# Kernel tuning notes

Measured on AMD Instinct MI355X. Metric: run time of the kernel, lower is better.

The kernel has to match this reference:

```python
import jax, jax.numpy as jnp
import numpy as np
from jax import lax

B, T, K = 8192, 512, 5


def setup_inputs() -> dict:
    key = jax.random.key(0)
    k1, k2, k3, k4 = jax.random.split(key, 4)
    potentials = jax.random.normal(k1, (B, T, K), dtype=jnp.float32)
    transition_params = jax.random.normal(k2, (K, K), dtype=jnp.float32) * 0.1
    sequence_lengths = jax.random.randint(k3, (B,), 1, T + 1, dtype=jnp.int32)
    tag_indices = jax.random.randint(k4, (B, T), 0, K, dtype=jnp.int32)
    return {
        "potentials": potentials,
        "transition_params": transition_params,
        "sequence_lengths": sequence_lengths,
        "tag_indices": tag_indices,
    }


def _crf(potentials, transition_params, sequence_lengths, tag_indices):
    Bn, Tn, Kn = potentials.shape
    alpha0 = potentials[:, 0]                        # (B, K)
    pots_rest = jnp.swapaxes(potentials[:, 1:], 0, 1)  # (T-1, B, K)
    ts = jnp.arange(1, Tn)
    valid = ts[:, None] < sequence_lengths[None, :]    # (T-1, B)
    tag_range = jnp.arange(Kn, dtype=jnp.int32)

    # ---- Viterbi forward: max-product DP with backpointers ----
    def vit_step(alpha, inp):
        pot_t, v = inp
        scores = alpha[:, :, None] + transition_params[None]  # (B, K, K) over prev i -> next j
        bp = jnp.argmax(scores, axis=1).astype(jnp.int32)     # (B, K)
        new_alpha = jnp.max(scores, axis=1) + pot_t
        alpha = jnp.where(v[:, None], new_alpha, alpha)       # freeze past seq end
        bp = jnp.where(v[:, None], bp, tag_range[None])       # identity bp past seq end
        return alpha, bp

    alpha_v, bps = lax.scan(vit_step, alpha0, (pots_rest, valid))
    last_tag = jnp.argmax(alpha_v, axis=1).astype(jnp.int32)  # (B,)

    # ---- backtrack ----
    def back_step(tag, bp_t):
        prev = jnp.take_along_axis(bp_t, tag[:, None], axis=1)[:, 0]
        return prev, prev

    _, prev_tags = lax.scan(back_step, last_tag, bps, reverse=True)  # (T-1, B) tags 0..T-2
    decoded = jnp.concatenate([jnp.swapaxes(prev_tags, 0, 1), last_tag[:, None]], axis=1)
    mask = jnp.arange(Tn)[None] < sequence_lengths[:, None]          # (B, T)
    decoded = jnp.where(mask, decoded, 0)

    # ---- forward algorithm: log partition ----
    def fwd_step(alpha, inp):
        pot_t, v = inp
        new_alpha = jax.nn.logsumexp(alpha[:, :, None] + transition_params[None], axis=1) + pot_t
        return jnp.where(v[:, None], new_alpha, alpha), None

    alpha_f, _ = lax.scan(fwd_step, alpha0, (pots_rest, valid))
    log_norm = jax.nn.logsumexp(alpha_f, axis=1)                     # (B,)

    # ---- gold sequence score ----
    unary = jnp.take_along_axis(potentials, tag_indices[:, :, None], axis=2)[:, :, 0]  # (B, T)
    unary = jnp.sum(jnp.where(mask, unary, 0.0), axis=1)
    trans_sc = transition_params[tag_indices[:, :-1], tag_indices[:, 1:]]              # (B, T-1)
    tmask = jnp.arange(1, Tn)[None] < sequence_lengths[:, None]
    binary = jnp.sum(jnp.where(tmask, trans_sc, 0.0), axis=1)

    log_likelihood = unary + binary - log_norm
    return decoded, log_likelihood


def reference(potentials, transition_params, sequence_lengths, tag_indices):
    return _crf(potentials, transition_params, sequence_lengths, tag_indices)
```

## Files before the change

kernel.cpp:

```cpp
#include <hip/hip_runtime.h>
#include <stdint.h>

#define KK 5
#define TT 512

template<int P> __device__ __forceinline__ float swzf(float v) {
  return __int_as_float(__builtin_amdgcn_ds_swizzle(__float_as_int(v), P));
}
template<int P> __device__ __forceinline__ int swzi(int v) {
  return __builtin_amdgcn_ds_swizzle(v, P);
}
#define BC0 0x018
#define BC1 0x038
#define BC2 0x058
#define BC3 0x078
#define BC4 0x098
#define X1 0x041F
#define X2 0x081F
#define X4 0x101F

__device__ __forceinline__ float sel5f(float v0,float v1,float v2,float v3,float v4,int ct){
  float u=v0; u=(ct==1)?v1:u; u=(ct==2)?v2:u; u=(ct==3)?v3:u; u=(ct==4)?v4:u; return u;
}
__device__ __forceinline__ uint32_t sel5u(uint32_t w0,uint32_t w1,uint32_t w2,uint32_t w3,uint32_t w4,int ct){
  uint32_t u=w0; u=(ct==1)?w1:u; u=(ct==2)?w2:u; u=(ct==3)?w3:u; u=(ct==4)?w4:u; return u;
}
__device__ __forceinline__ int telt(const int4 (&tp)[2], int s) {
  const int4 v = (s < 4) ? tp[0] : tp[1];
  const int m = s & 3;
  return m == 0 ? v.x : (m == 1 ? v.y : (m == 2 ? v.z : v.w));
}

__device__ __forceinline__ void loadCol(float (&d)[8], const float* __restrict__ colp, int k) {
  const int t0 = k * 8 + 1;
  if (k < TT / 8 - 1) {
#pragma unroll
    for (int s = 0; s < 8; ++s) d[s] = colp[(t0 + s) * KK];
  } else {
#pragma unroll
    for (int s = 0; s < 8; ++s) d[s] = colp[min(t0 + s, TT - 1) * KK];
  }
}
__device__ __forceinline__ void loadTag(int4 (&tp)[2], const int* __restrict__ tg, int k) {
  tp[0] = *(const int4*)(tg + 8 * k);
  tp[1] = *(const int4*)(tg + 8 * k + 4);
}

__global__ void sort_by_len(const int* __restrict__ lens, int* __restrict__ order, int B) {
  __shared__ int hist[513];
  __shared__ int off[513];
  const int tid = threadIdx.x;
  for (int i = tid; i < 513; i += 1024) hist[i] = 0;
  __syncthreads();
  for (int b = tid; b < B; b += 1024) atomicAdd(&hist[lens[b]], 1);
  __syncthreads();
  if (tid < 64) {
    int local[9];
    int sum = 0;
#pragma unroll
    for (int j = 0; j < 9; ++j) {
      const int i = tid * 9 + j;
      const int v = (i < 513) ? hist[i] : 0;
      local[j] = sum;
      sum += v;
    }
    int inc = sum;
#pragma unroll
    for (int d = 1; d < 64; d <<= 1) {
      const int n = __shfl_up(inc, d);
      inc += (tid >= d) ? n : 0;
    }
    const int excl = inc - sum;
#pragma unroll
    for (int j = 0; j < 9; ++j) {
      const int i = tid * 9 + j;
      if (i < 513) off[i] = excl + local[j];
    }
  }
  __syncthreads();
  for (int b = tid; b < B; b += 1024) {
    const int p = atomicAdd(&off[lens[b]], 1);
    order[B - 1 - p] = b;
  }
}

__device__ __forceinline__ void vit_map_block(const float (&pv)[8], int k, int len_eff,
                                              const float (&trc)[KK], float& a,
                                              int jj, int g, int r,
                                              uint32_t* __restrict__ s_map) {
  uint32_t bits = 0;
#pragma unroll
  for (int s = 0; s < 8; ++s) {
    const float av0 = swzf<BC0>(a), av1 = swzf<BC1>(a), av2 = swzf<BC2>(a),
                av3 = swzf<BC3>(a), av4 = swzf<BC4>(a);
    const float s0 = av0 + trc[0], s1 = av1 + trc[1], s2 = av2 + trc[2],
                s3 = av3 + trc[3], s4 = av4 + trc[4];
    const float bm = fmaxf(fmaxf(fmaxf(s0, s1), fmaxf(s2, s3)), s4);
    int bi = 4;
    bi = (s3 == bm) ? 3 : bi;
    bi = (s2 == bm) ? 2 : bi;
    bi = (s1 == bm) ? 1 : bi;
    bi = (s0 == bm) ? 0 : bi;
    const int t = k * 8 + s + 1;
    const bool act = (t < len_eff);
    a = act ? (bm + pv[s]) : a;
    const int bie = act ? bi : jj;
    bits |= (uint32_t)bie << (3 * s);
  }
  const uint32_t w0 = (uint32_t)__builtin_amdgcn_ds_bpermute(((g << 3) + 0) << 2, (int)bits);
  const uint32_t w1 = (uint32_t)__builtin_amdgcn_ds_bpermute(((g << 3) + 1) << 2, (int)bits);
  const uint32_t w2 = (uint32_t)__builtin_amdgcn_ds_bpermute(((g << 3) + 2) << 2, (int)bits);
  const uint32_t w3 = (uint32_t)__builtin_amdgcn_ds_bpermute(((g << 3) + 3) << 2, (int)bits);
  const uint32_t w4 = (uint32_t)__builtin_amdgcn_ds_bpermute(((g << 3) + 4) << 2, (int)bits);
  int cur = jj;
  uint32_t dec = 0;
#pragma unroll
  for (int s = 7; s >= 0; --s) {
    const uint32_t w = sel5u(w0, w1, w2, w3, w4, cur);
    const int b3 = (int)((w >> (3 * s)) & 7u);
    dec |= (uint32_t)b3 << (3 * s);
    cur = b3;
  }
  if (r < 5) s_map[g * 321 + k * 5 + jj] = dec;
}

__device__ __forceinline__ void fwd_blk(const float (&pv)[8], const int4 (&tp)[2],
                                        int k, int len, int len_eff,
                                        const float (&Wc)[KK], const float (&trcR)[KK],
                                        float& p, float& Cacc,
                                        float& pvcar, int& tagcar,
                                        float& usum, float& bsum, int r) {
#pragma unroll
  for (int s = 0; s < 8; ++s) {
    const float p0 = swzf<BC0>(p), p1 = swzf<BC1>(p), p2 = swzf<BC2>(p),
                p3 = swzf<BC3>(p), p4 = swzf<BC4>(p);
    const float u  = fmaf(p1, Wc[1], p0 * Wc[0]);
    const float v2 = fmaf(p3, Wc[3], p2 * Wc[2]);
    const float acc = fmaf(p4, Wc[4], u + v2);
    const float E = __expf(pv[s]);
    const int t = k * 8 + s + 1;
    const bool act = (t < len_eff);
    p = act ? (acc * E) : p;
  }
#pragma unroll
  for (int s2 = 0; s2 < 8; ++s2) {
    const int t = k * 8 + s2;
    const int ct = telt(tp, s2);
    const int pt = (s2 == 0) ? tagcar : telt(tp, s2 - 1);
    const float potv = (s2 == 0) ? pvcar : pv[s2 - 1];
    const bool um = (t < len) && (ct == r);
    usum += um ? potv : 0.0f;
    bsum += (um && t >= 1) ? sel5f(trcR[0], trcR[1], trcR[2], trcR[3], trcR[4], pt) : 0.0f;
  }
  pvcar = pv[7];
  tagcar = telt(tp, 7);
  float m = p;
  m = fmaxf(m, swzf<X1>(m));
  m = fmaxf(m, swzf<X2>(m));
  m = fmaxf(m, swzf<X4>(m));
  p *= (1.0f / m);
  Cacc += __logf(m);
}

__launch_bounds__(64)
__global__ void crf_kernel(const float* __restrict__ pot,
                           const float* __restrict__ trans,
                           const int* __restrict__ lens,
                           const int* __restrict__ tags,
                           const int* __restrict__ order,
                           float* __restrict__ out,
                           int B, int T) {
  __shared__ uint32_t s_map[8 * 321];
  __shared__ uint32_t s_chosen[8 * 65];
  const int lane = threadIdx.x;
  const int g = lane >> 3, r = lane & 7;
  const int jj = (r < 5) ? r : 4;
  const unsigned u = blockIdx.x;
  const int role = (u >> 3) & 1;
  const int idx = (int)((u & 7u) | ((u >> 4) << 3));
  const int b = order[idx * 8 + g];
  const int len = lens[b];
  const int len_eff = (r < 5) ? len : 0;
  const float* __restrict__ prow = pot + (size_t)b * (T * KK);
  const float* __restrict__ colp = prow + jj;

  int ml = len;
  ml = max(ml, __shfl_xor(ml, 8));
  ml = max(ml, __shfl_xor(ml, 16));
  ml = max(ml, __shfl_xor(ml, 32));
  const int nblk = (ml + 7) >> 3;

  if (role == 0) {
    float trc[KK];
#pragma unroll
    for (int i = 0; i < KK; ++i) trc[i] = trans[i * KK + jj];
    float a = (r < 5) ? prow[jj] : -3.0e38f;

    float pA[8], pB[8], pC[8];
    loadCol(pA, colp, 0);
    loadCol(pB, colp, min(1, nblk - 1));
    loadCol(pC, colp, min(2, nblk - 1));
    int blk = 0;
    while (true) {
      vit_map_block(pA, blk, len_eff, trc, a, jj, g, r, s_map);
      if (++blk == nblk) break;
      loadCol(pA, colp, min(blk + 2, nblk - 1));
      vit_map_block(pB, blk, len_eff, trc, a, jj, g, r, s_map);
      if (++blk == nblk) break;
      loadCol(pB, colp, min(blk + 2, nblk - 1));
      vit_map_block(pC, blk, len_eff, trc, a, jj, g, r, s_map);
      if (++blk == nblk) break;
      loadCol(pC, colp, min(blk + 2, nblk - 1));
    }
    float bm = a;
    bm = fmaxf(bm, swzf<X1>(bm));
    bm = fmaxf(bm, swzf<X2>(bm));
    bm = fmaxf(bm, swzf<X4>(bm));
    int cand = (r < 5 && a == bm) ? r : 7;
    cand = min(cand, swzi<X1>(cand));
    cand = min(cand, swzi<X2>(cand));
    cand = min(cand, swzi<X4>(cand));
    const int last = cand;

    if (r == 0) {
      int tag = last;
      for (int k2 = nblk - 1; k2 >= 0; --k2) {
        const uint32_t w = s_map[g * 321 + k2 * 5 + tag];
        s_chosen[g * 65 + k2] = w;
        tag = (int)(w & 7u);
      }
    }

    float* __restrict__ orow = out + (size_t)b * T;
#pragma unroll
    for (int kk = 0; kk < 8; ++kk) {
      const int k2 = kk * 8 + r;
      const uint32_t w = s_chosen[g * 65 + k2];
      const int base = k2 * 8;
      float f[8];
#pragma unroll
      for (int pI = 0; pI < 8; ++pI)
        f[pI] = (base + pI < len) ? (float)((w >> (3 * pI)) & 7u) : 0.0f;
      *(float4*)(orow + base)     = make_float4(f[0], f[1], f[2], f[3]);
      *(float4*)(orow + base + 4) = make_float4(f[4], f[5], f[6], f[7]);
    }

  } else {
    float Wc[KK], trcR[KK];
#pragma unroll
    for (int i = 0; i < KK; ++i) {
      trcR[i] = trans[i * KK + jj];
      Wc[i] = __expf(trcR[i]);
    }
    const float pj0 = prow[jj];
    float p = (r < 5) ? __expf(pj0) : 0.0f;
    float Cacc = 0.0f;
    float usum = 0.0f, bsum = 0.0f;
    float pvcar = pj0;
    int tagcar = 0;
    const int* __restrict__ tg = tags + (size_t)b * T;

    float pA[8], pB[8], pC[8];
    int4 TA[2], TB[2], TC[2];
    loadCol(pA, colp, 0);                loadTag(TA, tg, 0);
    loadCol(pB, colp, min(1, nblk - 1)); loadTag(TB, tg, min(1, nblk - 1));
    loadCol(pC, colp, min(2, nblk - 1)); loadTag(TC, tg, min(2, nblk - 1));
    int blk = 0;
    while (true) {
      fwd_blk(pA, TA, blk, len, len_eff, Wc, trcR, p, Cacc, pvcar, tagcar, usum, bsum, r);
      if (++blk == nblk) break;
      loadCol(pA, colp, min(blk + 2, nblk - 1)); loadTag(TA, tg, min(blk + 2, nblk - 1));
      fwd_blk(pB, TB, blk, len, len_eff, Wc, trcR, p, Cacc, pvcar, tagcar, usum, bsum, r);
      if (++blk == nblk) break;
      loadCol(pB, colp, min(blk + 2, nblk - 1)); loadTag(TB, tg, min(blk + 2, nblk - 1));
      fwd_blk(pC, TC, blk, len, len_eff, Wc, trcR, p, Cacc, pvcar, tagcar, usum, bsum, r);
      if (++blk == nblk) break;
      loadCol(pC, colp, min(blk + 2, nblk - 1)); loadTag(TC, tg, min(blk + 2, nblk - 1));
    }
    float sc = usum + bsum;
    sc += swzf<X1>(sc);
    sc += swzf<X2>(sc);
    sc += swzf<X4>(sc);
    float ps = p;
    ps += swzf<X1>(ps);
    ps += swzf<X2>(ps);
    ps += swzf<X4>(ps);
    const float logZ = Cacc + __logf(ps);
    if (r == 0) out[(size_t)B * T + b] = sc - logZ;
  }
}

extern "C" void kernel_launch(void* const* d_in, const int* in_sizes, int n_in,
                              void* d_out, int out_size, void* d_ws, size_t ws_size,
                              hipStream_t stream) {
  const float* pot   = (const float*)d_in[0];
  const float* trans = (const float*)d_in[1];
  const int*   lens  = (const int*)d_in[2];
  const int*   tags  = (const int*)d_in[3];
  float* out = (float*)d_out;

  const int B = in_sizes[2];
  const int T = in_sizes[3] / B;

  int* order = (int*)d_ws;

  sort_by_len<<<1, 1024, 0, stream>>>(lens, order, B);

  const int nblocks = 2 * (B / 8);
  crf_kernel<<<nblocks, 64, 0, stream>>>(pot, trans, lens, tags, order, out, B, T);
}
```

Measured before the change: 90.88 us.

## Fuse Viterbi and forward-algorithm recurrences into a single wavefront per sequence group

Merges the two roles (Viterbi max-product and forward logsumexp plus gold score) that used to run in separate blocks into one block doing both recurrences in the same time-step loop. Potentials and tags are loaded once instead of twice, and the two independent dependency chains are interleaved to hide swizzle and ALU latency. The grid halves to B/8 blocks, so there is less parallelism and more register pressure per wave.

```diff
diff --git a/kernel.cpp b/kernel.cpp
--- a/kernel.cpp
+++ b/kernel.cpp
@@ -84,15 +84,21 @@
   }
 }
 
-__device__ __forceinline__ void vit_map_block(const float (&pv)[8], int k, int len_eff,
-                                              const float (&trc)[KK], float& a,
-                                              int jj, int g, int r,
-                                              uint32_t* __restrict__ s_map) {
+__device__ __forceinline__ void vf_block(const float (&pv)[8], const int4 (&tp)[2],
+    int k, int len, int len_eff,
+    const float (&trc)[KK], const float (&Wc)[KK],
+    float& aV, float& p, float& Cacc,
+    float& pvcar, int& tagcar, float& usum, float& bsum,
+    int jj, int g, int r, uint32_t* __restrict__ s_map) {
   uint32_t bits = 0;
 #pragma unroll
   for (int s = 0; s < 8; ++s) {
-    const float av0 = swzf<BC0>(a), av1 = swzf<BC1>(a), av2 = swzf<BC2>(a),
-                av3 = swzf<BC3>(a), av4 = swzf<BC4>(a);
+    const float av0 = swzf<BC0>(aV), av1 = swzf<BC1>(aV), av2 = swzf<BC2>(aV),
+                av3 = swzf<BC3>(aV), av4 = swzf<BC4>(aV);
+    const float q0 = swzf<BC0>(p), q1 = swzf<BC1>(p), q2 = swzf<BC2>(p),
+                q3 = swzf<BC3>(p), q4 = swzf<BC4>(p);
+    const int t = k * 8 + s + 1;
+    const bool act = (t < len_eff);
     const float s0 = av0 + trc[0], s1 = av1 + trc[1], s2 = av2 + trc[2],
                 s3 = av3 + trc[3], s4 = av4 + trc[4];
     const float bm = fmaxf(fmaxf(fmaxf(s0, s1), fmaxf(s2, s3)), s4);
@@ -101,12 +107,27 @@
     bi = (s2 == bm) ? 2 : bi;
     bi = (s1 == bm) ? 1 : bi;
     bi = (s0 == bm) ? 0 : bi;
-    const int t = k * 8 + s + 1;
-    const bool act = (t < len_eff);
-    a = act ? (bm + pv[s]) : a;
+    aV = act ? (bm + pv[s]) : aV;
     const int bie = act ? bi : jj;
     bits |= (uint32_t)bie << (3 * s);
-  }
+    const float uacc = fmaf(q1, Wc[1], q0 * Wc[0]);
+    const float v2 = fmaf(q3, Wc[3], q2 * Wc[2]);
+    const float acc = fmaf(q4, Wc[4], uacc + v2);
+    const float E = __expf(pv[s]);
+    p = act ? (acc * E) : p;
+  }
+#pragma unroll
+  for (int s2 = 0; s2 < 8; ++s2) {
+    const int t = k * 8 + s2;
+    const int ct = telt(tp, s2);
+    const int pt = (s2 == 0) ? tagcar : telt(tp, s2 - 1);
+    const float potv = (s2 == 0) ? pvcar : pv[s2 - 1];
+    const bool um = (t < len) && (ct == r);
+    usum += um ? potv : 0.0f;
+    bsum += (um && t >= 1) ? sel5f(trc[0], trc[1], trc[2], trc[3], trc[4], pt) : 0.0f;
+  }
+  pvcar = pv[7];
+  tagcar = telt(tp, 7);
   const uint32_t w0 = (uint32_t)__builtin_amdgcn_ds_bpermute(((g << 3) + 0) << 2, (int)bits);
   const uint32_t w1 = (uint32_t)__builtin_amdgcn_ds_bpermute(((g << 3) + 1) << 2, (int)bits);
   const uint32_t w2 = (uint32_t)__builtin_amdgcn_ds_bpermute(((g << 3) + 2) << 2, (int)bits);
@@ -122,38 +143,6 @@
     cur = b3;
   }
   if (r < 5) s_map[g * 321 + k * 5 + jj] = dec;
-}
-
-__device__ __forceinline__ void fwd_blk(const float (&pv)[8], const int4 (&tp)[2],
-                                        int k, int len, int len_eff,
-                                        const float (&Wc)[KK], const float (&trcR)[KK],
-                                        float& p, float& Cacc,
-                                        float& pvcar, int& tagcar,
-                                        float& usum, float& bsum, int r) {
-#pragma unroll
-  for (int s = 0; s < 8; ++s) {
-    const float p0 = swzf<BC0>(p), p1 = swzf<BC1>(p), p2 = swzf<BC2>(p),
-                p3 = swzf<BC3>(p), p4 = swzf<BC4>(p);
-    const float u  = fmaf(p1, Wc[1], p0 * Wc[0]);
-    const float v2 = fmaf(p3, Wc[3], p2 * Wc[2]);
-    const float acc = fmaf(p4, Wc[4], u + v2);
-    const float E = __expf(pv[s]);
-    const int t = k * 8 + s + 1;
-    const bool act = (t < len_eff);
-    p = act ? (acc * E) : p;
-  }
-#pragma unroll
-  for (int s2 = 0; s2 < 8; ++s2) {
-    const int t = k * 8 + s2;
-    const int ct = telt(tp, s2);
-    const int pt = (s2 == 0) ? tagcar : telt(tp, s2 - 1);
-    const float potv = (s2 == 0) ? pvcar : pv[s2 - 1];
-    const bool um = (t < len) && (ct == r);
-    usum += um ? potv : 0.0f;
-    bsum += (um && t >= 1) ? sel5f(trcR[0], trcR[1], trcR[2], trcR[3], trcR[4], pt) : 0.0f;
-  }
-  pvcar = pv[7];
-  tagcar = telt(tp, 7);
   float m = p;
   m = fmaxf(m, swzf<X1>(m));
   m = fmaxf(m, swzf<X2>(m));
@@ -175,10 +164,7 @@
   const int lane = threadIdx.x;
   const int g = lane >> 3, r = lane & 7;
   const int jj = (r < 5) ? r : 4;
-  const unsigned u = blockIdx.x;
-  const int role = (u >> 3) & 1;
-  const int idx = (int)((u & 7u) | ((u >> 4) << 3));
-  const int b = order[idx * 8 + g];
+  const int b = order[blockIdx.x * 8 + g];
   const int len = lens[b];
   const int len_eff = (r < 5) ? len : 0;
   const float* __restrict__ prow = pot + (size_t)b * (T * KK);
@@ -190,103 +176,80 @@
   ml = max(ml, __shfl_xor(ml, 32));
   const int nblk = (ml + 7) >> 3;
 
-  if (role == 0) {
-    float trc[KK];
-#pragma unroll
-    for (int i = 0; i < KK; ++i) trc[i] = trans[i * KK + jj];
-    float a = (r < 5) ? prow[jj] : -3.0e38f;
-
-    float pA[8], pB[8], pC[8];
-    loadCol(pA, colp, 0);
-    loadCol(pB, colp, min(1, nblk - 1));
-    loadCol(pC, colp, min(2, nblk - 1));
-    int blk = 0;
-    while (true) {
-      vit_map_block(pA, blk, len_eff, trc, a, jj, g, r, s_map);
-      if (++blk == nblk) break;
-      loadCol(pA, colp, min(blk + 2, nblk - 1));
-      vit_map_block(pB, blk, len_eff, trc, a, jj, g, r, s_map);
-      if (++blk == nblk) break;
-      loadCol(pB, colp, min(blk + 2, nblk - 1));
-      vit_map_block(pC, blk, len_eff, trc, a, jj, g, r, s_map);
-      if (++blk == nblk) break;
-      loadCol(pC, colp, min(blk + 2, nblk - 1));
-    }
-    float bm = a;
-    bm = fmaxf(bm, swzf<X1>(bm));
-    bm = fmaxf(bm, swzf<X2>(bm));
-    bm = fmaxf(bm, swzf<X4>(bm));
-    int cand = (r < 5 && a == bm) ? r : 7;
-    cand = min(cand, swzi<X1>(cand));
-    cand = min(cand, swzi<X2>(cand));
-    cand = min(cand, swzi<X4>(cand));
-    const int last = cand;
-
-    if (r == 0) {
-      int tag = last;
-      for (int k2 = nblk - 1; k2 >= 0; --k2) {
-        const uint32_t w = s_map[g * 321 + k2 * 5 + tag];
-        s_chosen[g * 65 + k2] = w;
-        tag = (int)(w & 7u);
-      }
-    }
-
-    float* __restrict__ orow = out + (size_t)b * T;
-#pragma unroll
-    for (int kk = 0; kk < 8; ++kk) {
-      const int k2 = kk * 8 + r;
-      const uint32_t w = s_chosen[g * 65 + k2];
-      const int base = k2 * 8;
-      float f[8];
-#pragma unroll
-      for (int pI = 0; pI < 8; ++pI)
-        f[pI] = (base + pI < len) ? (float)((w >> (3 * pI)) & 7u) : 0.0f;
-      *(float4*)(orow + base)     = make_float4(f[0], f[1], f[2], f[3]);
-      *(float4*)(orow + base + 4) = make_float4(f[4], f[5], f[6], f[7]);
-    }
-
-  } else {
-    float Wc[KK], trcR[KK];
-#pragma unroll
-    for (int i = 0; i < KK; ++i) {
-      trcR[i] = trans[i * KK + jj];
-      Wc[i] = __expf(trcR[i]);
-    }
-    const float pj0 = prow[jj];
-    float p = (r < 5) ? __expf(pj0) : 0.0f;
-    float Cacc = 0.0f;
-    float usum = 0.0f, bsum = 0.0f;
-    float pvcar = pj0;
-    int tagcar = 0;
-    const int* __restrict__ tg = tags + (size_t)b * T;
-
-    float pA[8], pB[8], pC[8];
-    int4 TA[2], TB[2], TC[2];
-    loadCol(pA, colp, 0);                loadTag(TA, tg, 0);
-    loadCol(pB, colp, min(1, nblk - 1)); loadTag(TB, tg, min(1, nblk - 1));
-    loadCol(pC, colp, min(2, nblk - 1)); loadTag(TC, tg, min(2, nblk - 1));
-    int blk = 0;
-    while (true) {
-      fwd_blk(pA, TA, blk, len, len_eff, Wc, trcR, p, Cacc, pvcar, tagcar, usum, bsum, r);
-      if (++blk == nblk) break;
-      loadCol(pA, colp, min(blk + 2, nblk - 1)); loadTag(TA, tg, min(blk + 2, nblk - 1));
-      fwd_blk(pB, TB, blk, len, len_eff, Wc, trcR, p, Cacc, pvcar, tagcar, usum, bsum, r);
-      if (++blk == nblk) break;
-      loadCol(pB, colp, min(blk + 2, nblk - 1)); loadTag(TB, tg, min(blk + 2, nblk - 1));
-      fwd_blk(pC, TC, blk, len, len_eff, Wc, trcR, p, Cacc, pvcar, tagcar, usum, bsum, r);
-      if (++blk == nblk) break;
-      loadCol(pC, colp, min(blk + 2, nblk - 1)); loadTag(TC, tg, min(blk + 2, nblk - 1));
-    }
-    float sc = usum + bsum;
-    sc += swzf<X1>(sc);
-    sc += swzf<X2>(sc);
-    sc += swzf<X4>(sc);
-    float ps = p;
-    ps += swzf<X1>(ps);
-    ps += swzf<X2>(ps);
-    ps += swzf<X4>(ps);
-    const float logZ = Cacc + __logf(ps);
-    if (r == 0) out[(size_t)B * T + b] = sc - logZ;
+  float trc[KK], Wc[KK];
+#pragma unroll
+  for (int i = 0; i < KK; ++i) {
+    trc[i] = trans[i * KK + jj];
+    Wc[i] = __expf(trc[i]);
+  }
+  const float pj0 = prow[jj];
+  float aV = (r < 5) ? pj0 : -3.0e38f;
+  float p = (r < 5) ? __expf(pj0) : 0.0f;
+  float Cacc = 0.0f, usum = 0.0f, bsum = 0.0f;
+  float pvcar = pj0;
+  int tagcar = 0;
+  const int* __restrict__ tg = tags + (size_t)b * T;
+
+  float pA[8], pB[8], pC[8];
+  int4 TA[2], TB[2], TC[2];
+  loadCol(pA, colp, 0);                loadTag(TA, tg, 0);
+  loadCol(pB, colp, min(1, nblk - 1)); loadTag(TB, tg, min(1, nblk - 1));
+  loadCol(pC, colp, min(2, nblk - 1)); loadTag(TC, tg, min(2, nblk - 1));
+  int blk = 0;
+  while (true) {
+    vf_block(pA, TA, blk, len, len_eff, trc, Wc, aV, p, Cacc, pvcar, tagcar, usum, bsum, jj, g, r, s_map);
+    if (++blk == nblk) break;
+    loadCol(pA, colp, min(blk + 2, nblk - 1)); loadTag(TA, tg, min(blk + 2, nblk - 1));
+    vf_block(pB, TB, blk, len, len_eff, trc, Wc, aV, p, Cacc, pvcar, tagcar, usum, bsum, jj, g, r, s_map);
+    if (++blk == nblk) break;
+    loadCol(pB, colp, min(blk + 2, nblk - 1)); loadTag(TB, tg, min(blk + 2, nblk - 1));
+    vf_block(pC, TC, blk, len, len_eff, trc, Wc, aV, p, Cacc, pvcar, tagcar, usum, bsum, jj, g, r, s_map);
+    if (++blk == nblk) break;
+    loadCol(pC, colp, min(blk + 2, nblk - 1)); loadTag(TC, tg, min(blk + 2, nblk - 1));
+  }
+
+  float bm = aV;
+  bm = fmaxf(bm, swzf<X1>(bm));
+  bm = fmaxf(bm, swzf<X2>(bm));
+  bm = fmaxf(bm, swzf<X4>(bm));
+  int cand = (r < 5 && aV == bm) ? r : 7;
+  cand = min(cand, swzi<X1>(cand));
+  cand = min(cand, swzi<X2>(cand));
+  cand = min(cand, swzi<X4>(cand));
+  const int last = cand;
+
+  float sc = usum + bsum;
+  sc += swzf<X1>(sc);
+  sc += swzf<X2>(sc);
+  sc += swzf<X4>(sc);
+  float ps = p;
+  ps += swzf<X1>(ps);
+  ps += swzf<X2>(ps);
+  ps += swzf<X4>(ps);
+  const float logZ = Cacc + __logf(ps);
+  if (r == 1) out[(size_t)B * T + b] = sc - logZ;
+
+  if (r == 0) {
+    int tag = last;
+    for (int k2 = nblk - 1; k2 >= 0; --k2) {
+      const uint32_t w = s_map[g * 321 + k2 * 5 + tag];
+      s_chosen[g * 65 + k2] = w;
+      tag = (int)(w & 7u);
+    }
+  }
+
+  float* __restrict__ orow = out + (size_t)b * T;
+#pragma unroll
+  for (int kk = 0; kk < 8; ++kk) {
+    const int k2 = kk * 8 + r;
+    const uint32_t w = s_chosen[g * 65 + k2];
+    const int base = k2 * 8;
+    float f[8];
+#pragma unroll
+    for (int pI = 0; pI < 8; ++pI)
+      f[pI] = (base + pI < len) ? (float)((w >> (3 * pI)) & 7u) : 0.0f;
+    *(float4*)(orow + base)     = make_float4(f[0], f[1], f[2], f[3]);
+    *(float4*)(orow + base + 4) = make_float4(f[4], f[5], f[6], f[7]);
   }
 }
 
@@ -306,6 +269,5 @@
 
   sort_by_len<<<1, 1024, 0, stream>>>(lens, order, B);
 
-  const int nblocks = 2 * (B / 8);
-  crf_kernel<<<nblocks, 64, 0, stream>>>(pot, trans, lens, tags, order, out, B, T);
-}
+  crf_kernel<<<B / 8, 64, 0, stream>>>(pot, trans, lens, tags, order, out, B, T);
+}
```

New measurement: 146.8 us. +61.5%, slower.
